# Performance work log

Hardware: AMD Instinct MI355X
Metric: run time of the kernel (lower is better)

The kernel has to match this reference:

```python
import jax, jax.numpy as jnp
import numpy as np

B, S, D = 2, 2048, 2048
H = 16
Q_LORA, KV_LORA = 1536, 512
D_NOPE, D_ROPE = 128, 64
D_QK = D_NOPE + D_ROPE  # 192
D_V = 128
EPS = 1e-6
SCALE = D_QK ** -0.5


def rms_norm(x, w):
    var = jnp.mean(jnp.square(x), axis=-1, keepdims=True)
    return x * jax.lax.rsqrt(var + EPS) * w


def apply_rotary_emb(x, freqs_cis):
    # x: [B, S, h, dr]; freqs_cis: [S, dr//2, 2] (cos, sin); interleaved pairs
    b, s, h, dr = x.shape
    xp = x.reshape(b, s, h, dr // 2, 2)
    x0, x1 = xp[..., 0], xp[..., 1]
    cos = freqs_cis[None, :, None, :, 0]
    sin = freqs_cis[None, :, None, :, 1]
    o0 = x0 * cos - x1 * sin
    o1 = x0 * sin + x1 * cos
    return jnp.stack([o0, o1], axis=-1).reshape(b, s, h, dr)


def setup_inputs() -> dict:
    key = jax.random.key(0)
    ks = jax.random.split(key, 8)
    std = 0.02
    x = jax.random.normal(ks[0], (B, S, D), jnp.float32)
    inv_freq = 1.0 / (10000.0 ** (np.arange(0, D_ROPE, 2, dtype=np.float32) / D_ROPE))
    ang = np.outer(np.arange(S, dtype=np.float32), inv_freq)  # [S, 32]
    freqs_cis = jnp.asarray(np.stack([np.cos(ang), np.sin(ang)], axis=-1))
    return {
        'x': x,
        'freqs_cis': freqs_cis,
        'Wqa': jax.random.normal(ks[1], (Q_LORA, D), jnp.float32) * std,
        'q_a_ln_w': jnp.ones((Q_LORA,), jnp.float32),
        'Wqb': jax.random.normal(ks[2], (H * D_QK, Q_LORA), jnp.float32) * std,
        'Wkva': jax.random.normal(ks[3], (KV_LORA + D_ROPE, D), jnp.float32) * std,
        'kv_a_ln_w': jnp.ones((KV_LORA,), jnp.float32),
        'Wkvb': jax.random.normal(ks[4], (H * (D_NOPE + D_V), KV_LORA), jnp.float32) * std,
        'Wo': jax.random.normal(ks[5], (D, H * D_V), jnp.float32) * std,
    }


def reference(x, freqs_cis, Wqa, q_a_ln_w, Wqb, Wkva, kv_a_ln_w, Wkvb, Wo):
    # Low-rank Q projection: down -> RMSNorm -> up
    q = rms_norm(jnp.einsum('bsd,rd->bsr', x, Wqa), q_a_ln_w)
    q = jnp.einsum('bsr,er->bse', q, Wqb).reshape(B, S, H, D_QK)
    q_nope, q_pe = q[..., :D_NOPE], q[..., D_NOPE:]
    q = jnp.concatenate([q_nope, apply_rotary_emb(q_pe, freqs_cis)], axis=-1)

    # Low-rank KV projection with shared (MQA) rope part
    kv = jnp.einsum('bsd,ed->bse', x, Wkva)
    kv_c, k_pe = kv[..., :KV_LORA], kv[..., KV_LORA:]
    kv_c = rms_norm(kv_c, kv_a_ln_w)
    k_pe = apply_rotary_emb(k_pe[:, :, None, :], freqs_cis)  # [B,S,1,D_ROPE]
    kv = jnp.einsum('bsr,er->bse', kv_c, Wkvb).reshape(B, S, H, D_NOPE + D_V)
    k_nope, v = kv[..., :D_NOPE], kv[..., D_NOPE:]
    k = jnp.concatenate(
        [k_nope, jnp.broadcast_to(k_pe, (B, S, H, D_ROPE))], axis=-1)

    # Causal SDPA with scale = qk_head_dim ** -0.5
    scores = jnp.einsum('bqhd,bkhd->bhqk', q, k) * SCALE
    causal = jnp.tril(jnp.ones((S, S), bool))
    scores = jnp.where(causal[None, None], scores, jnp.finfo(scores.dtype).min)
    probs = jax.nn.softmax(scores, axis=-1)
    out = jnp.einsum('bhqk,bkhd->bqhd', probs, v).reshape(B, S, H * D_V)
    return jnp.einsum('bse,de->bsd', out, Wo)
```

## Files before the change

kernel.cpp:

```cpp
#include <hip/hip_runtime.h>
#include <math.h>

#define B_ 2
#define S_ 2048
#define D_ 2048
#define H_ 16
#define QLORA 1536
#define KVLORA 512
#define DN 128
#define DR 64
#define DQK 192
#define DV 128
#define EPSF 1e-6f
#define SCALEF 0.07216878364870322f

typedef short short8 __attribute__((ext_vector_type(8)));
typedef float float4v __attribute__((ext_vector_type(4)));

__device__ __forceinline__ unsigned short f2bf(float f) {
    union { float f; unsigned u; } x; x.f = f;
    unsigned r = x.u + 0x7fffu + ((x.u >> 16) & 1u);
    return (unsigned short)(r >> 16);
}
__device__ __forceinline__ float bf2f(unsigned short u) {
    union { unsigned u; float f; } x; x.u = (unsigned)u << 16;
    return x.f;
}

#define GLD16(src, dst)                                                        \
    __builtin_amdgcn_global_load_lds(                                          \
        (const __attribute__((address_space(1))) void*)(src),                  \
        (__attribute__((address_space(3))) void*)(dst), 16, 0, 0)

__global__ __launch_bounds__(256) void conv_all(
        const float* __restrict__ s0, unsigned short* __restrict__ d0, long e0,
        const float* __restrict__ s1, unsigned short* __restrict__ d1, long e1,
        const float* __restrict__ s2, unsigned short* __restrict__ d2, long e2,
        const float* __restrict__ s3, unsigned short* __restrict__ d3, long e3,
        const float* __restrict__ s4, unsigned short* __restrict__ d4, long e4,
        const float* __restrict__ s5, unsigned short* __restrict__ d5) {
    long c = (long)blockIdx.x * 256 + threadIdx.x;
    const float* src;
    unsigned short* dst;
    if      (c < e0) { src = s0; dst = d0; }
    else if (c < e1) { src = s1; dst = d1; c -= e0; }
    else if (c < e2) { src = s2; dst = d2; c -= e1; }
    else if (c < e3) { src = s3; dst = d3; c -= e2; }
    else if (c < e4) { src = s4; dst = d4; c -= e3; }
    else             { src = s5; dst = d5; c -= e4; }
    const float* p = src + c * 8;
    float4 a = *(const float4*)(p);
    float4 b = *(const float4*)(p + 4);
    union { short8 v; unsigned short u[8]; } t;
    t.u[0] = f2bf(a.x); t.u[1] = f2bf(a.y); t.u[2] = f2bf(a.z); t.u[3] = f2bf(a.w);
    t.u[4] = f2bf(b.x); t.u[5] = f2bf(b.y); t.u[6] = f2bf(b.z); t.u[7] = f2bf(b.w);
    *(short8*)&dst[c * 8] = t.v;
}

#define GBM 128
#define GBN 128
#define GBK 64

template <typename OT>
__global__ __launch_bounds__(256) void gemm_t(const unsigned short* __restrict__ A,
                                              const unsigned short* __restrict__ W,
                                              OT* __restrict__ C,
                                              int M, int N, int K) {
    __shared__ unsigned short As[GBM * GBK];
    __shared__ unsigned short Ws[GBN * GBK];

    const int tid = threadIdx.x;
    const int w = tid >> 6, lane = tid & 63;
    const int l16 = lane & 15, quad = lane >> 4;
    const int wm = (w >> 1) * 64, wn = (w & 1) * 64;
    const int row0 = blockIdx.y * GBM, col0 = blockIdx.x * GBN;

    const int rL  = lane >> 3;
    const int c8g = (lane & 7) ^ rL;
    const int swzk[2] = { (((0 * 4) + quad) ^ (l16 & 7)) * 8,
                          (((1 * 4) + quad) ^ (l16 & 7)) * 8 };

    const float4v zf = {0.f, 0.f, 0.f, 0.f};
    float4v acc[4][4] = {{zf, zf, zf, zf}, {zf, zf, zf, zf},
                         {zf, zf, zf, zf}, {zf, zf, zf, zf}};

    for (int k0 = 0; k0 < K; k0 += GBK) {
        __syncthreads();
#pragma unroll
        for (int j = 0; j < 4; ++j) {
            const int ch = w * 4 + j;
            const int r = ch * 8 + rL;
            GLD16(&A[(size_t)(row0 + r) * K + k0 + c8g * 8], &As[ch * 512]);
            GLD16(&W[(size_t)(col0 + r) * K + k0 + c8g * 8], &Ws[ch * 512]);
        }
        __syncthreads();

#pragma unroll
        for (int kk = 0; kk < 2; ++kk) {
            const int swz = swzk[kk];
            short8 af[4], bf[4];
#pragma unroll
            for (int mi = 0; mi < 4; ++mi)
                af[mi] = *(const short8*)&As[(wm + mi * 16 + l16) * GBK + swz];
#pragma unroll
            for (int ni = 0; ni < 4; ++ni)
                bf[ni] = *(const short8*)&Ws[(wn + ni * 16 + l16) * GBK + swz];
#pragma unroll
            for (int mi = 0; mi < 4; ++mi)
#pragma unroll
                for (int ni = 0; ni < 4; ++ni)
                    acc[mi][ni] = __builtin_amdgcn_mfma_f32_16x16x32_bf16(af[mi], bf[ni], acc[mi][ni], 0, 0, 0);
        }
    }

#pragma unroll
    for (int mi = 0; mi < 4; ++mi)
#pragma unroll
        for (int ni = 0; ni < 4; ++ni)
#pragma unroll
            for (int r = 0; r < 4; ++r) {
                size_t idx = (size_t)(row0 + wm + mi * 16 + quad * 4 + r) * N + col0 + wn + ni * 16 + l16;
                if constexpr (sizeof(OT) == 2) C[idx] = f2bf(acc[mi][ni][r]);
                else                           C[idx] = acc[mi][ni][r];
            }
}

__global__ __launch_bounds__(256) void rmsnorm_b(const float* __restrict__ X,
                                                 const float* __restrict__ w,
                                                 unsigned short* __restrict__ Y,
                                                 int n, int ld) {
    __shared__ float tmp[4];
    const int row = blockIdx.x;
    const int tid = threadIdx.x;
    const float* x = X + (size_t)row * ld;

    float ss = 0.f;
    for (int c = tid; c < n; c += 256) {
        float v = x[c];
        ss = fmaf(v, v, ss);
    }
#pragma unroll
    for (int off = 32; off; off >>= 1) ss += __shfl_xor(ss, off, 64);
    if ((tid & 63) == 0) tmp[tid >> 6] = ss;
    __syncthreads();
    ss = tmp[0] + tmp[1] + tmp[2] + tmp[3];
    float r = rsqrtf(ss / (float)n + EPSF);

    for (int c = tid; c < n; c += 256)
        Y[(size_t)row * n + c] = f2bf(x[c] * r * w[c]);
}

__global__ __launch_bounds__(256) void kv_post(const float* __restrict__ KV,
                                               const float* __restrict__ w,
                                               const float* __restrict__ fc,
                                               unsigned short* __restrict__ kvcb,
                                               float* __restrict__ kpe,
                                               int ldkv) {
    __shared__ float tmp[4];
    const int row = blockIdx.x;
    const int s = row & (S_ - 1);
    const int tid = threadIdx.x;
    const float* kv = KV + (size_t)row * ldkv;

    float ss = 0.f;
#pragma unroll
    for (int c = tid; c < KVLORA; c += 256) {
        float v = kv[c];
        ss = fmaf(v, v, ss);
    }
#pragma unroll
    for (int off = 32; off; off >>= 1) ss += __shfl_xor(ss, off, 64);
    if ((tid & 63) == 0) tmp[tid >> 6] = ss;
    __syncthreads();
    ss = tmp[0] + tmp[1] + tmp[2] + tmp[3];
    float r = rsqrtf(ss / (float)KVLORA + EPSF);

#pragma unroll
    for (int c = tid; c < KVLORA; c += 256)
        kvcb[(size_t)row * KVLORA + c] = f2bf(kv[c] * r * w[c]);

    if (tid < 32) {
        int i = tid;
        float c0 = fc[(s * 32 + i) * 2 + 0];
        float s0 = fc[(s * 32 + i) * 2 + 1];
        float x0 = kv[KVLORA + 2 * i];
        float x1 = kv[KVLORA + 2 * i + 1];
        kpe[(size_t)row * DR + 2 * i]     = x0 * c0 - x1 * s0;
        kpe[(size_t)row * DR + 2 * i + 1] = x0 * s0 + x1 * c0;
    }
}

__global__ __launch_bounds__(256) void pack_k(const unsigned short* __restrict__ kvbb,
                                              const float* __restrict__ kpe,
                                              unsigned short* __restrict__ Kbf) {
    const int c = blockIdx.x * 256 + threadIdx.x;
    const int total = B_ * H_ * S_ * (DQK / 8);
    if (c >= total) return;
    const int d8 = c % (DQK / 8);
    const int hs = c / (DQK / 8);
    const int s  = hs % S_;
    const int bh = hs / S_;
    const int b  = bh / H_;
    const int h  = bh % H_;
    const int d  = d8 * 8;
    const int row = b * S_ + s;

    short8 v;
    if (d < DN) {
        v = *(const short8*)&kvbb[(size_t)row * (H_ * 256) + h * 256 + d];
    } else {
        const float* src = kpe + (size_t)row * DR + (d - DN);
        float4 a = *(const float4*)(src);
        float4 bb = *(const float4*)(src + 4);
        union { short8 v; unsigned short u[8]; } t;
        t.u[0] = f2bf(a.x);  t.u[1] = f2bf(a.y);  t.u[2] = f2bf(a.z);  t.u[3] = f2bf(a.w);
        t.u[4] = f2bf(bb.x); t.u[5] = f2bf(bb.y); t.u[6] = f2bf(bb.z); t.u[7] = f2bf(bb.w);
        v = t.v;
    }
    *(short8*)&Kbf[(size_t)c * 8] = v;
}

__global__ __launch_bounds__(256) void pack_vt(const unsigned short* __restrict__ kvbb,
                                               unsigned short* __restrict__ Vt) {
    __shared__ unsigned short T[DV][72];
    const int st = blockIdx.x;
    const int bh = blockIdx.y;
    const int b = bh >> 4, h = bh & 15;
    const int s0 = st * 64;
    const int tid = threadIdx.x;

    for (int c = tid; c < 64 * 16; c += 256) {
        int sp = c >> 4, ch = c & 15;
        short8 v = *(const short8*)&kvbb[(size_t)(b * S_ + s0 + sp) * (H_ * 256) + h * 256 + DN + ch * 8];
        union { short8 v; unsigned short u[8]; } t; t.v = v;
        int dv = ch * 8;
#pragma unroll
        for (int e = 0; e < 8; ++e) T[dv + e][sp] = t.u[e];
    }
    __syncthreads();
    for (int c = tid; c < 128 * 8; c += 256) {
        int dv = c >> 3, ch = c & 7;
        *(short8*)&Vt[((size_t)bh * DV + dv) * S_ + s0 + ch * 8] = *(short8*)&T[dv][ch * 8];
    }
}

#define KROW 200
#define VROW 72
#define PROW 72
#define NQT 32

__global__ __launch_bounds__(256, 2) void flash_mfma(const unsigned short* __restrict__ Qb,
                                                     const float* __restrict__ fc,
                                                     const unsigned short* __restrict__ Kbf,
                                                     const unsigned short* __restrict__ Vt,
                                                     unsigned short* __restrict__ Ob) {
    __shared__ unsigned short Ks[64][KROW];
    __shared__ unsigned short Vs[DV][VROW];
    __shared__ unsigned short Ps[4][16][PROW];

    const int bh = blockIdx.x;
    const int bx = blockIdx.y;
    const int b = bh >> 4, h = bh & 15;
    const int tid = threadIdx.x;
    const int w = tid >> 6, lane = tid & 63;
    const int l16 = lane & 15, quad = lane >> 4;

    const unsigned short* Kg = Kbf + (size_t)bh * S_ * DQK;
    const unsigned short* Vg = Vt + (size_t)bh * DV * S_;

    for (int half = 0; half < 2; ++half) {
        const int qt = half ? (NQT - 1 - bx) : bx;
        const int q0 = qt * 64;
        const int ntiles = qt + 1;
        const int s = q0 + w * 16 + l16;

        short8 a_q[6];
        {
            const unsigned short* qrow = Qb + (size_t)(b * S_ + s) * (H_ * DQK) + h * DQK;
#pragma unroll
            for (int i = 0; i < 6; ++i) {
                short8 t = *(const short8*)&qrow[i * 32 + quad * 8];
                if (i >= 4) {
                    union { short8 v; unsigned short u[8]; } x; x.v = t;
#pragma unroll
                    for (int j = 0; j < 4; ++j) {
                        int ip = (i - 4) * 16 + quad * 4 + j;
                        float c0 = fc[(s * 32 + ip) * 2 + 0];
                        float s0 = fc[(s * 32 + ip) * 2 + 1];
                        float x0 = bf2f(x.u[2 * j]);
                        float x1 = bf2f(x.u[2 * j + 1]);
                        x.u[2 * j]     = f2bf(x0 * c0 - x1 * s0);
                        x.u[2 * j + 1] = f2bf(x0 * s0 + x1 * c0);
                    }
                    t = x.v;
                }
                a_q[i] = t;
            }
        }

        const float4v zf = {0.f, 0.f, 0.f, 0.f};
        float4v o_acc[8] = {zf, zf, zf, zf, zf, zf, zf, zf};
        float l_r[4] = {0.f, 0.f, 0.f, 0.f};

        short8 ldK[6], ldV[4];
#pragma unroll
        for (int i = 0; i < 6; ++i) {
            int c = tid + i * 256;
            int r = c / 24, cc = c % 24;
            ldK[i] = *(const short8*)&Kg[(size_t)r * DQK + cc * 8];
        }
#pragma unroll
        for (int i = 0; i < 4; ++i) {
            int c = tid + i * 256;
            int r = c >> 3, cc = c & 7;
            ldV[i] = *(const short8*)&Vg[(size_t)r * S_ + cc * 8];
        }

        for (int kt = 0; kt < ntiles; ++kt) {
            const int kbase = kt * 64;
            __syncthreads();
#pragma unroll
            for (int i = 0; i < 6; ++i) {
                int c = tid + i * 256;
                int r = c / 24, cc = c % 24;
                *(short8*)&Ks[r][cc * 8] = ldK[i];
            }
#pragma unroll
            for (int i = 0; i < 4; ++i) {
                int c = tid + i * 256;
                int r = c >> 3, cc = c & 7;
                *(short8*)&Vs[r][cc * 8] = ldV[i];
            }
            if (kt + 1 < ntiles) {
                const int kb2 = kbase + 64;
#pragma unroll
                for (int i = 0; i < 6; ++i) {
                    int c = tid + i * 256;
                    int r = c / 24, cc = c % 24;
                    ldK[i] = *(const short8*)&Kg[(size_t)(kb2 + r) * DQK + cc * 8];
                }
#pragma unroll
                for (int i = 0; i < 4; ++i) {
                    int c = tid + i * 256;
                    int r = c >> 3, cc = c & 7;
                    ldV[i] = *(const short8*)&Vg[(size_t)r * S_ + kb2 + cc * 8];
                }
            }
            __syncthreads();

            float4v sc[4] = {zf, zf, zf, zf};
#pragma unroll
            for (int kg = 0; kg < 4; ++kg) {
#pragma unroll
                for (int i = 0; i < 6; ++i) {
                    short8 bk = *(const short8*)&Ks[kg * 16 + l16][i * 32 + quad * 8];
                    sc[kg] = __builtin_amdgcn_mfma_f32_16x16x32_bf16(a_q[i], bk, sc[kg], 0, 0, 0);
                }
            }

            const bool last = (kt == ntiles - 1);
#pragma unroll
            for (int kg = 0; kg < 4; ++kg) {
                int key = kbase + kg * 16 + l16;
#pragma unroll
                for (int r = 0; r < 4; ++r) {
                    float sv = sc[kg][r] * SCALEF;
                    if (last && key > q0 + w * 16 + quad * 4 + r) sv = -1e30f;
                    float p = __expf(sv);
                    l_r[r] += p;
                    Ps[w][quad * 4 + r][kg * 16 + l16] = f2bf(p);
                }
            }

            __syncthreads();

#pragma unroll
            for (int kc = 0; kc < 2; ++kc) {
                short8 pa = *(const short8*)&Ps[w][l16][kc * 32 + quad * 8];
#pragma unroll
                for (int dvt = 0; dvt < 8; ++dvt) {
                    short8 vb = *(const short8*)&Vs[dvt * 16 + l16][kc * 32 + quad * 8];
                    o_acc[dvt] = __builtin_amdgcn_mfma_f32_16x16x32_bf16(pa, vb, o_acc[dvt], 0, 0, 0);
                }
            }
        }

#pragma unroll
        for (int r = 0; r < 4; ++r) {
            float t = l_r[r];
            t += __shfl_xor(t, 1);
            t += __shfl_xor(t, 2);
            t += __shfl_xor(t, 4);
            t += __shfl_xor(t, 8);
            l_r[r] = t;
        }
#pragma unroll
        for (int r = 0; r < 4; ++r) {
            float inv = 1.f / l_r[r];
            int row = q0 + w * 16 + quad * 4 + r;
            unsigned short* op = Ob + (size_t)(b * S_ + row) * (H_ * DV) + h * DV;
#pragma unroll
            for (int dvt = 0; dvt < 8; ++dvt)
                op[dvt * 16 + l16] = f2bf(o_acc[dvt][r] * inv);
        }
    }
}

extern "C" void kernel_launch(void* const* d_in, const int* in_sizes, int n_in,
                              void* d_out, int out_size, void* d_ws, size_t ws_size,
                              hipStream_t stream) {
    const float* x    = (const float*)d_in[0];
    const float* fc   = (const float*)d_in[1];
    const float* Wqa  = (const float*)d_in[2];
    const float* qlw  = (const float*)d_in[3];
    const float* Wqb  = (const float*)d_in[4];
    const float* Wkva = (const float*)d_in[5];
    const float* kvw  = (const float*)d_in[6];
    const float* Wkvb = (const float*)d_in[7];
    const float* Wo   = (const float*)d_in[8];
    float* out = (float*)d_out;

    const int M = B_ * S_;
    const int NQKV = QLORA + 640;
    char* wsb = (char*)d_ws;

    unsigned short* qb  = (unsigned short*)wsb;
    unsigned short* Wob = (unsigned short*)(wsb + 25165824);
    char* R2 = wsb + 50331648;
    float*          qlkv  = (float*)R2;
    unsigned short* xb    = (unsigned short*)(R2 + 35651584);
    unsigned short* Wcat  = (unsigned short*)(R2 + 52428800);
    unsigned short* kvbb  = (unsigned short*)R2;
    unsigned short* attnb = (unsigned short*)R2;
    char* R3 = R2 + 67108864;
    unsigned short* qlatb = (unsigned short*)R3;
    unsigned short* Wqbb  = (unsigned short*)(R3 + 12582912);
    unsigned short* Kbf   = (unsigned short*)R3;
    char* R4 = R3 + 25165824;
    float*          kpe   = (float*)R4;
    unsigned short* kvcb  = (unsigned short*)(R4 + 1048576);
    unsigned short* Wkvbb = (unsigned short*)(R4 + 5242880);
    unsigned short* Vt    = (unsigned short*)R4;

    {
        const long e0 = 1048576;
        const long e1 = e0 + 393216;
        const long e2 = e1 + 147456;
        const long e3 = e2 + 589824;
        const long e4 = e3 + 262144;
        const long tot = e4 + 524288;
        conv_all<<<(int)(tot / 256), 256, 0, stream>>>(
            x, xb, e0,
            Wqa, Wcat, e1,
            Wkva, Wcat + (size_t)QLORA * D_, e2,
            Wqb, Wqbb, e3,
            Wkvb, Wkvbb, e4,
            Wo, Wob);
    }

    gemm_t<float><<<dim3(NQKV / GBN, M / GBM), 256, 0, stream>>>(xb, Wcat, qlkv, M, NQKV, D_);

    rmsnorm_b<<<M, 256, 0, stream>>>(qlkv, qlw, qlatb, QLORA, NQKV);
    kv_post<<<M, 256, 0, stream>>>(qlkv + QLORA, kvw, fc, kvcb, kpe, NQKV);

    gemm_t<unsigned short><<<dim3(H_ * DQK / GBN, M / GBM), 256, 0, stream>>>(qlatb, Wqbb, qb, M, H_ * DQK, QLORA);
    gemm_t<unsigned short><<<dim3(H_ * 256 / GBN, M / GBM), 256, 0, stream>>>(kvcb, Wkvbb, kvbb, M, H_ * 256, KVLORA);

    {
        int total = B_ * H_ * S_ * (DQK / 8);
        pack_k<<<(total + 255) / 256, 256, 0, stream>>>(kvbb, kpe, Kbf);
        pack_vt<<<dim3(S_ / 64, B_ * H_), 256, 0, stream>>>(kvbb, Vt);
    }

    flash_mfma<<<dim3(B_ * H_, NQT / 2), 256, 0, stream>>>(qb, fc, Kbf, Vt, attnb);

    gemm_t<float><<<dim3(D_ / GBN, M / GBM), 256, 0, stream>>>(attnb, Wob, out, M, D_, D_);
}
```

Before: 460.4 us.

## Enlarge flash attention query tile and double-buffer swizzled K/V via direct LDS loads

```diff
diff --git a/kernel.cpp b/kernel.cpp
--- a/kernel.cpp
+++ b/kernel.cpp
@@ -244,19 +244,16 @@
     }
 }
 
-#define KROW 200
-#define VROW 72
-#define PROW 72
-#define NQT 32
-
-__global__ __launch_bounds__(256, 2) void flash_mfma(const unsigned short* __restrict__ Qb,
+#define QTILES 16
+
+__global__ __launch_bounds__(256, 1) void flash_mfma(const unsigned short* __restrict__ Qb,
                                                      const float* __restrict__ fc,
                                                      const unsigned short* __restrict__ Kbf,
                                                      const unsigned short* __restrict__ Vt,
                                                      unsigned short* __restrict__ Ob) {
-    __shared__ unsigned short Ks[64][KROW];
-    __shared__ unsigned short Vs[DV][VROW];
-    __shared__ unsigned short Ps[4][16][PROW];
+    __shared__ unsigned short Ks[2][64 * 192];
+    __shared__ unsigned short Vs[2][128 * 64];
+    __shared__ unsigned short Ps[4][32][72];
 
     const int bh = blockIdx.x;
     const int bx = blockIdx.y;
@@ -264,18 +261,41 @@
     const int tid = threadIdx.x;
     const int w = tid >> 6, lane = tid & 63;
     const int l16 = lane & 15, quad = lane >> 4;
+    const int sw = l16 & 7;
 
     const unsigned short* Kg = Kbf + (size_t)bh * S_ * DQK;
     const unsigned short* Vg = Vt + (size_t)bh * DV * S_;
 
+    auto stage = [&](int kt_, int bufi) {
+        const int kb_ = kt_ * 64;
+#pragma unroll
+        for (int i_ = 0; i_ < 6; ++i_) {
+            int ch = (w * 6 + i_) * 64 + lane;
+            int r_ = ch / 24, c_ = ch - r_ * 24;
+            GLD16(&Kg[(size_t)(kb_ + r_) * DQK + ((c_ ^ (r_ & 7)) << 3)],
+                  &Ks[bufi][(w * 6 + i_) * 512]);
+        }
+#pragma unroll
+        for (int i_ = 0; i_ < 4; ++i_) {
+            int ch = (w * 4 + i_) * 64 + lane;
+            int r_ = ch >> 3, c_ = ch & 7;
+            GLD16(&Vg[(size_t)r_ * S_ + kb_ + ((c_ ^ (r_ & 7)) << 3)],
+                  &Vs[bufi][(w * 4 + i_) * 512]);
+        }
+    };
+
     for (int half = 0; half < 2; ++half) {
-        const int qt = half ? (NQT - 1 - bx) : bx;
-        const int q0 = qt * 64;
-        const int ntiles = qt + 1;
-        const int s = q0 + w * 16 + l16;
-
-        short8 a_q[6];
-        {
+        const int qt = half ? (QTILES - 1 - bx) : bx;
+        const int q0 = qt * 128;
+        const int ntiles = 2 * qt + 2;
+        const int wr0 = q0 + w * 32;
+
+        stage(0, 0);
+
+        short8 a_q[2][6];
+#pragma unroll
+        for (int g = 0; g < 2; ++g) {
+            const int s = wr0 + g * 16 + l16;
             const unsigned short* qrow = Qb + (size_t)(b * S_ + s) * (H_ * DQK) + h * DQK;
 #pragma unroll
             for (int i = 0; i < 6; ++i) {
@@ -294,115 +314,102 @@
                     }
                     t = x.v;
                 }
-                a_q[i] = t;
+                a_q[g][i] = t;
             }
         }
 
         const float4v zf = {0.f, 0.f, 0.f, 0.f};
-        float4v o_acc[8] = {zf, zf, zf, zf, zf, zf, zf, zf};
-        float l_r[4] = {0.f, 0.f, 0.f, 0.f};
-
-        short8 ldK[6], ldV[4];
-#pragma unroll
-        for (int i = 0; i < 6; ++i) {
-            int c = tid + i * 256;
-            int r = c / 24, cc = c % 24;
-            ldK[i] = *(const short8*)&Kg[(size_t)r * DQK + cc * 8];
-        }
-#pragma unroll
-        for (int i = 0; i < 4; ++i) {
-            int c = tid + i * 256;
-            int r = c >> 3, cc = c & 7;
-            ldV[i] = *(const short8*)&Vg[(size_t)r * S_ + cc * 8];
-        }
-
+        float4v o_acc[2][8] = {{zf, zf, zf, zf, zf, zf, zf, zf},
+                               {zf, zf, zf, zf, zf, zf, zf, zf}};
+        float l_r[2][4] = {{0.f, 0.f, 0.f, 0.f}, {0.f, 0.f, 0.f, 0.f}};
+
+        int buf = 0;
         for (int kt = 0; kt < ntiles; ++kt) {
-            const int kbase = kt * 64;
-            __syncthreads();
-#pragma unroll
-            for (int i = 0; i < 6; ++i) {
-                int c = tid + i * 256;
-                int r = c / 24, cc = c % 24;
-                *(short8*)&Ks[r][cc * 8] = ldK[i];
-            }
-#pragma unroll
-            for (int i = 0; i < 4; ++i) {
-                int c = tid + i * 256;
-                int r = c >> 3, cc = c & 7;
-                *(short8*)&Vs[r][cc * 8] = ldV[i];
-            }
+            const int kb = kt * 64;
+
+            __builtin_amdgcn_s_barrier();
             if (kt + 1 < ntiles) {
-                const int kb2 = kbase + 64;
+                stage(kt + 1, buf ^ 1);
+                asm volatile("s_waitcnt vmcnt(10)" ::: "memory");
+            } else {
+                asm volatile("s_waitcnt vmcnt(0)" ::: "memory");
+            }
+            __builtin_amdgcn_sched_barrier(0);
+            __builtin_amdgcn_s_barrier();
+            __builtin_amdgcn_sched_barrier(0);
+
+            if (kb <= wr0 + 31) {
+                const unsigned short* Kb_ = Ks[buf];
+                const unsigned short* Vb_ = Vs[buf];
+
+                float4v sc[2][4] = {{zf, zf, zf, zf}, {zf, zf, zf, zf}};
 #pragma unroll
                 for (int i = 0; i < 6; ++i) {
-                    int c = tid + i * 256;
-                    int r = c / 24, cc = c % 24;
-                    ldK[i] = *(const short8*)&Kg[(size_t)(kb2 + r) * DQK + cc * 8];
+                    short8 bk[4];
+#pragma unroll
+                    for (int kg = 0; kg < 4; ++kg)
+                        bk[kg] = *(const short8*)&Kb_[(kg * 16 + l16) * 192 + (((i * 4 + quad) ^ sw) << 3)];
+#pragma unroll
+                    for (int kg = 0; kg < 4; ++kg) {
+                        sc[0][kg] = __builtin_amdgcn_mfma_f32_16x16x32_bf16(a_q[0][i], bk[kg], sc[0][kg], 0, 0, 0);
+                        sc[1][kg] = __builtin_amdgcn_mfma_f32_16x16x32_bf16(a_q[1][i], bk[kg], sc[1][kg], 0, 0, 0);
+                    }
                 }
-#pragma unroll
-                for (int i = 0; i < 4; ++i) {
-                    int c = tid + i * 256;
-                    int r = c >> 3, cc = c & 7;
-                    ldV[i] = *(const short8*)&Vg[(size_t)r * S_ + kb2 + cc * 8];
+
+#pragma unroll
+                for (int g = 0; g < 2; ++g) {
+                    const int rg0 = wr0 + g * 16;
+                    const bool mneed = (kb + 63 > rg0);
+#pragma unroll
+                    for (int kg = 0; kg < 4; ++kg) {
+                        const int key = kb + kg * 16 + l16;
+#pragma unroll
+                        for (int r = 0; r < 4; ++r) {
+                            float p = __expf(sc[g][kg][r] * SCALEF);
+                            if (mneed && key > rg0 + quad * 4 + r) p = 0.f;
+                            l_r[g][r] += p;
+                            Ps[w][g * 16 + quad * 4 + r][kg * 16 + l16] = f2bf(p);
+                        }
+                    }
                 }
-            }
-            __syncthreads();
-
-            float4v sc[4] = {zf, zf, zf, zf};
-#pragma unroll
-            for (int kg = 0; kg < 4; ++kg) {
-#pragma unroll
-                for (int i = 0; i < 6; ++i) {
-                    short8 bk = *(const short8*)&Ks[kg * 16 + l16][i * 32 + quad * 8];
-                    sc[kg] = __builtin_amdgcn_mfma_f32_16x16x32_bf16(a_q[i], bk, sc[kg], 0, 0, 0);
+
+#pragma unroll
+                for (int kc = 0; kc < 2; ++kc) {
+                    short8 pa0 = *(const short8*)&Ps[w][l16][kc * 32 + quad * 8];
+                    short8 pa1 = *(const short8*)&Ps[w][16 + l16][kc * 32 + quad * 8];
+#pragma unroll
+                    for (int dvt = 0; dvt < 8; ++dvt) {
+                        short8 vb = *(const short8*)&Vb_[(dvt * 16 + l16) * 64 + (((kc * 4 + quad) ^ sw) << 3)];
+                        o_acc[0][dvt] = __builtin_amdgcn_mfma_f32_16x16x32_bf16(pa0, vb, o_acc[0][dvt], 0, 0, 0);
+                        o_acc[1][dvt] = __builtin_amdgcn_mfma_f32_16x16x32_bf16(pa1, vb, o_acc[1][dvt], 0, 0, 0);
+                    }
                 }
             }
-
-            const bool last = (kt == ntiles - 1);
-#pragma unroll
-            for (int kg = 0; kg < 4; ++kg) {
-                int key = kbase + kg * 16 + l16;
-#pragma unroll
-                for (int r = 0; r < 4; ++r) {
-                    float sv = sc[kg][r] * SCALEF;
-                    if (last && key > q0 + w * 16 + quad * 4 + r) sv = -1e30f;
-                    float p = __expf(sv);
-                    l_r[r] += p;
-                    Ps[w][quad * 4 + r][kg * 16 + l16] = f2bf(p);
-                }
-            }
-
-            __syncthreads();
-
-#pragma unroll
-            for (int kc = 0; kc < 2; ++kc) {
-                short8 pa = *(const short8*)&Ps[w][l16][kc * 32 + quad * 8];
-#pragma unroll
-                for (int dvt = 0; dvt < 8; ++dvt) {
-                    short8 vb = *(const short8*)&Vs[dvt * 16 + l16][kc * 32 + quad * 8];
-                    o_acc[dvt] = __builtin_amdgcn_mfma_f32_16x16x32_bf16(pa, vb, o_acc[dvt], 0, 0, 0);
-                }
-            }
-        }
-
-#pragma unroll
-        for (int r = 0; r < 4; ++r) {
-            float t = l_r[r];
-            t += __shfl_xor(t, 1);
-            t += __shfl_xor(t, 2);
-            t += __shfl_xor(t, 4);
-            t += __shfl_xor(t, 8);
-            l_r[r] = t;
-        }
-#pragma unroll
-        for (int r = 0; r < 4; ++r) {
-            float inv = 1.f / l_r[r];
-            int row = q0 + w * 16 + quad * 4 + r;
-            unsigned short* op = Ob + (size_t)(b * S_ + row) * (H_ * DV) + h * DV;
-#pragma unroll
-            for (int dvt = 0; dvt < 8; ++dvt)
-                op[dvt * 16 + l16] = f2bf(o_acc[dvt][r] * inv);
-        }
+            buf ^= 1;
+        }
+
+#pragma unroll
+        for (int g = 0; g < 2; ++g)
+#pragma unroll
+            for (int r = 0; r < 4; ++r) {
+                float t = l_r[g][r];
+                t += __shfl_xor(t, 1);
+                t += __shfl_xor(t, 2);
+                t += __shfl_xor(t, 4);
+                t += __shfl_xor(t, 8);
+                l_r[g][r] = t;
+            }
+#pragma unroll
+        for (int g = 0; g < 2; ++g)
+#pragma unroll
+            for (int r = 0; r < 4; ++r) {
+                float inv = 1.f / l_r[g][r];
+                int row = wr0 + g * 16 + quad * 4 + r;
+                unsigned short* op = Ob + (size_t)(b * S_ + row) * (H_ * DV) + h * DV;
+#pragma unroll
+                for (int dvt = 0; dvt < 8; ++dvt)
+                    op[dvt * 16 + l16] = f2bf(o_acc[g][dvt][r] * inv);
+            }
     }
 }
 
@@ -472,7 +479,7 @@
         pack_vt<<<dim3(S_ / 64, B_ * H_), 256, 0, stream>>>(kvbb, Vt);
     }
 
-    flash_mfma<<<dim3(B_ * H_, NQT / 2), 256, 0, stream>>>(qb, fc, Kbf, Vt, attnb);
+    flash_mfma<<<dim3(B_ * H_, QTILES / 2), 256, 0, stream>>>(qb, fc, Kbf, Vt, attnb);
 
     gemm_t<float><<<dim3(D_ / GBN, M / GBM), 256, 0, stream>>>(attnb, Wob, out, M, D_, D_);
 }
```

Measured after the change: 466.5 us. Within noise of the previous version (+1.3%).
